# Kernel tuning notes

Measured on AMD Instinct MI355X. Metric: run time of the kernel, lower is better.

Reference implementation:

```python
import jax, jax.numpy as jnp
import numpy as np

B = 65536      # batch
E = 4          # experts per node
F = 32         # per-node input features
H = 256        # hidden width
NODES = 4
D_MID = 128    # intermediate node output dim
D_OUT = 8      # final head dim


def _lin_w(k, fan_in, fan_out):
    b = 1.0 / np.sqrt(fan_in)
    return jax.random.uniform(k, (E, fan_in, fan_out), jnp.float32, -b, b)


def setup_inputs() -> dict:
    key = jax.random.key(0)
    ks = jax.random.split(key, 8)
    feats = jax.random.normal(ks[0], (B, NODES * F), dtype=jnp.float32)
    # routing one-hot blocks embedded in the input vector (as the module expects)
    ohs = [jax.nn.one_hot(jax.random.randint(ks[1 + j], (B,), 0, E), E, dtype=jnp.float32)
           for j in range(NODES)]
    input_val = jnp.concatenate([feats] + ohs, axis=1)  # [B, 144]
    p = {"input_val": input_val}
    kc = iter(jax.random.split(ks[5], 32))
    # node 0: no pre-interface; post: F->H relu, H->D_MID relu
    p["W0_0"] = _lin_w(next(kc), F, H); p["b0_0"] = jnp.full((E, H), 0.1, jnp.float32)
    p["W0_1"] = _lin_w(next(kc), H, D_MID); p["b0_1"] = jnp.full((E, D_MID), 0.1, jnp.float32)
    # nodes 1,2: pre F->H relu; post (D_MID+H)->H relu, H->D_MID relu
    for j in (1, 2):
        p[f"W{j}_pre"] = _lin_w(next(kc), F, H); p[f"b{j}_pre"] = jnp.full((E, H), 0.1, jnp.float32)
        p[f"W{j}_0"] = _lin_w(next(kc), D_MID + H, H); p[f"b{j}_0"] = jnp.full((E, H), 0.1, jnp.float32)
        p[f"W{j}_1"] = _lin_w(next(kc), H, D_MID); p[f"b{j}_1"] = jnp.full((E, D_MID), 0.1, jnp.float32)
    # node 3 (output): pre F->H relu; post (D_MID+H)->H relu, H->D_OUT identity
    p["W3_pre"] = _lin_w(next(kc), F, H); p["b3_pre"] = jnp.full((E, H), 0.1, jnp.float32)
    p["W3_0"] = _lin_w(next(kc), D_MID + H, H); p["b3_0"] = jnp.full((E, H), 0.1, jnp.float32)
    p["W3_1"] = jax.random.uniform(next(kc), (E, H, D_OUT), jnp.float32, -0.003, 0.003)
    p["b3_1"] = jax.random.uniform(next(kc), (E, D_OUT), jnp.float32, -0.003, 0.003)
    return p


def reference(input_val, W0_0, b0_0, W0_1, b0_1,
              W1_pre, b1_pre, W1_0, b1_0, W1_1, b1_1,
              W2_pre, b2_pre, W2_0, b2_0, W2_1, b2_1,
              W3_pre, b3_pre, W3_0, b3_0, W3_1, b3_1):
    relu = jax.nn.relu
    xs = [input_val[:, j * F:(j + 1) * F] for j in range(NODES)]          # per-node features
    ohs = [input_val[:, NODES * F + j * E: NODES * F + (j + 1) * E] for j in range(NODES)]

    def combine(oh, outs):  # oh [B,E] exact one-hot; outs [E,B,D] -> exact per-row expert pick
        return jnp.einsum('be,ebo->bo', oh, outs)

    # node 0 (no previous-level input)
    def n0(W0, b0, W1, b1):
        h = relu(xs[0] @ W0 + b0)
        return relu(h @ W1 + b1)
    x = combine(ohs[0], jax.vmap(n0)(W0_0, b0_0, W0_1, b0_1))  # [B, D_MID]

    def node(xj, xprev, relu_last):
        def f(Wp, bp, W0, b0, W1, b1):
            h = relu(xj @ Wp + bp)                      # pre-interface
            h = jnp.concatenate([xprev, h], axis=-1)    # interface: cat(prev, pre)
            h = relu(h @ W0 + b0)
            o = h @ W1 + b1
            return relu(o) if relu_last else o
        return f

    x = combine(ohs[1], jax.vmap(node(xs[1], x, True))(W1_pre, b1_pre, W1_0, b1_0, W1_1, b1_1))
    x = combine(ohs[2], jax.vmap(node(xs[2], x, True))(W2_pre, b2_pre, W2_0, b2_0, W2_1, b2_1))
    x = combine(ohs[3], jax.vmap(node(xs[3], x, False))(W3_pre, b3_pre, W3_0, b3_0, W3_1, b3_1))
    return x  # [B, D_OUT]
```

## Files before the change

kernel.cpp:

```cpp
#include <hip/hip_runtime.h>
#include <hip/hip_bf16.h>
#include <stdint.h>

typedef unsigned int u32;
typedef unsigned short u16;
typedef unsigned char u8;
typedef __bf16 bf16x8 __attribute__((ext_vector_type(8)));
typedef float f32x4 __attribute__((ext_vector_type(4)));

#define NB 65536
#define NBLK 1280
#define PERM_TOT (NBLK * 64)
#define INVR 0xFFFFFFFFu
#define BLK_DEAD 0xFFFFu

#define O_ROWS 0
#define O_XJ   256
#define O_P    (O_XJ + 4096)
#define O_H    (O_P + 16384)
#define O_RED  O_P
#define SM_BYTES (O_H + 32768)

__device__ __host__ constexpr int TS(int m) {
  constexpr int t[12] = {0, 64, 320, 384, 1152, 1408, 1472, 2240, 2496, 2560, 3328, 3360};
  return t[m];
}

__device__ __forceinline__ u16 f2bf(float f) {
  u32 u = __builtin_bit_cast(u32, f);
  u32 r = (u + 0x7FFFu + ((u >> 16) & 1u)) >> 16;
  return (u16)r;
}
__device__ __forceinline__ float relu_f(float x) { return x > 0.f ? x : 0.f; }
__device__ __forceinline__ f32x4 mfma16(bf16x8 a, bf16x8 b, f32x4 c) {
  return __builtin_amdgcn_mfma_f32_16x16x32_bf16(a, b, c, 0, 0, 0);
}

__device__ __forceinline__ void mkpair(f32x4 acc, float bias, bool dorelu, int l16,
                                       u32& w0, u32& w1) {
  float v0 = acc[0] + bias, v1 = acc[1] + bias, v2 = acc[2] + bias, v3 = acc[3] + bias;
  if (dorelu) { v0 = relu_f(v0); v1 = relu_f(v1); v2 = relu_f(v2); v3 = relu_f(v3); }
  u32 a = (u32)f2bf(v0) | ((u32)f2bf(v1) << 16);
  u32 b = (u32)f2bf(v2) | ((u32)f2bf(v3) << 16);
  u32 ax = (u32)__shfl_xor((int)a, 1);
  u32 bx = (u32)__shfl_xor((int)b, 1);
  if ((l16 & 1) == 0) { w0 = (a & 0xffffu) | (ax << 16); w1 = (a >> 16) | (ax & 0xffff0000u); }
  else                { w0 = (bx & 0xffffu) | (b << 16); w1 = (bx >> 16) | (b & 0xffff0000u); }
}

__device__ __forceinline__ void frag_store_pair(char* base, int KT, int m0, int col,
                                                u32 w0, u32 w1) {
  char* d = base + (((m0 >> 4) * KT + (col >> 5)) << 10) +
            (((m0 & 15) + (((col & 31) >> 3) << 4)) << 4) + (col & 7) * 2;
  *(u32*)d = w0; *(u32*)(d + 16) = w1;
}


__global__ void k_init(u32* cnt) { cnt[threadIdx.x] = 0u; }

__global__ void k_route(const float* __restrict__ inp, u8* __restrict__ bkt,
                        u32* __restrict__ cnt) {
  __shared__ u32 h[256];
  const int tid = threadIdx.x;
  h[tid] = 0u;
  __syncthreads();
  const int r = blockIdx.x * 256 + tid;
  const float4* oh = (const float4*)(inp + (size_t)r * 144 + 128);
  u32 b = 0;
#pragma unroll
  for (int j = 0; j < 4; j++) {
    float4 v = oh[j];
    u32 e = v.y > 0.5f ? 1u : (v.z > 0.5f ? 2u : (v.w > 0.5f ? 3u : 0u));
    b |= e << (2 * j);
  }
  bkt[r] = (u8)b;
  atomicAdd(&h[b], 1u);
  __syncthreads();
  atomicAdd(&cnt[tid], h[tid]);
}

__global__ void k_scan(const u32* __restrict__ cnt, u32* __restrict__ cur,
                       u16* __restrict__ blk2b, u32* __restrict__ perm) {
  __shared__ u32 s[256];
  const int tid = threadIdx.x;
  const u32 c = cnt[tid];
  const u32 pad = (c + 63u) & ~63u;
  s[tid] = pad;
  __syncthreads();
  for (int d = 1; d < 256; d <<= 1) {
    u32 v = (tid >= d) ? s[tid - d] : 0u;
    __syncthreads();
    s[tid] += v;
    __syncthreads();
  }
  const u32 off = s[tid] - pad;
  const u32 total = s[255];
  cur[tid] = off;
  for (u32 i = off + c; i < off + pad; i++) perm[i] = INVR;
  for (u32 blk = off >> 6; blk < (off + pad) >> 6; blk++) blk2b[blk] = (u16)tid;
  for (u32 i = total + tid; i < PERM_TOT; i += 256) perm[i] = INVR;
  for (u32 blk = (total >> 6) + tid; blk < NBLK; blk += 256) blk2b[blk] = BLK_DEAD;
}

__global__ void k_scatter(const u8* __restrict__ bkt, u32* __restrict__ cur,
                          u32* __restrict__ perm) {
  __shared__ u32 h[256], base[256];
  const int tid = threadIdx.x;
  h[tid] = 0u;
  __syncthreads();
  const int r = blockIdx.x * 256 + tid;
  const u32 b = bkt[r];
  const u32 rank = atomicAdd(&h[b], 1u);
  __syncthreads();
  base[tid] = h[tid] ? atomicAdd(&cur[tid], h[tid]) : 0u;
  __syncthreads();
  perm[base[b] + rank] = (u32)r;
}


struct PrepArgs {
  const float* src[11];
  int K[11], Nsrc[11];
  int tileStart[12];
};

__global__ void k_prep(__bf16* __restrict__ pk, PrepArgs pa) {
  const int tid = threadIdx.x;
  const int gt = blockIdx.x * 4 + (tid >> 6);
  const int lane = tid & 63, quad = lane >> 4, l16 = lane & 15;
  int m = 0;
  while (gt >= pa.tileStart[m + 1]) m++;
  const int loc = gt - pa.tileStart[m];
  const int K = pa.K[m], Ns = pa.Nsrc[m];
  const int Np = Ns < 16 ? 16 : Ns;
  const int KT = K >> 5, NT = Np >> 4;
  const int e = loc / (KT * NT), rem = loc % (KT * NT);
  const int nt = rem / KT, kt = rem % KT;
  const int k = kt * 32 + quad * 8, n = nt * 16 + l16;
  u32 hw[4];
  if (n < Ns) {
    const float* s = pa.src[m] + ((size_t)e * K + k) * Ns + n;
    u16 h[8];
#pragma unroll
    for (int j = 0; j < 8; j++) h[j] = f2bf(s[(size_t)j * Ns]);
    hw[0] = (u32)h[0] | ((u32)h[1] << 16);
    hw[1] = (u32)h[2] | ((u32)h[3] << 16);
    hw[2] = (u32)h[4] | ((u32)h[5] << 16);
    hw[3] = (u32)h[6] | ((u32)h[7] << 16);
  } else {
    hw[0] = hw[1] = hw[2] = hw[3] = 0u;
  }
  uint4 w; w.x = hw[0]; w.y = hw[1]; w.z = hw[2]; w.w = hw[3];
  *(uint4*)((char*)pk + (size_t)gt * 1024 + lane * 16) = w;
}


__device__ __forceinline__ void xj_load(const float* inp, u32 myrow, int tid, int node,
                                        float4& v0, float4& v1) {
  v0 = make_float4(0.f, 0.f, 0.f, 0.f); v1 = v0;
  if (myrow != INVR) {
    const int c8 = (tid & 3) << 3;
    const float4* p = (const float4*)(inp + (size_t)myrow * 144 + node * 32 + c8);
    v0 = p[0]; v1 = p[1];
  }
}

__device__ __forceinline__ void xj_store(char* sm, int tid, float4 v0, float4 v1) {
  const int r = tid >> 2;
  uint4 w;
  w.x = (u32)f2bf(v0.x) | ((u32)f2bf(v0.y) << 16);
  w.y = (u32)f2bf(v0.z) | ((u32)f2bf(v0.w) << 16);
  w.z = (u32)f2bf(v1.x) | ((u32)f2bf(v1.y) << 16);
  w.w = (u32)f2bf(v1.z) | ((u32)f2bf(v1.w) << 16);
  *(uint4*)(sm + O_XJ + ((r >> 4) << 10) + ((((tid & 3) << 4) + (r & 15)) << 4)) = w;
}

__device__ __forceinline__ void pre_gemm(char* sm, u32 e, int wave, int lane,
                                         const __bf16* Wp, const float* bp) {
  const int l16 = lane & 15;
  const int wn0 = wave * 64;
  const int rsel = ((lane >> 4) << 2) + ((l16 & 1) ? 2 : 0);
  const int colp = l16 & ~1;
  float bias[4];
#pragma unroll
  for (int nt = 0; nt < 4; nt++) bias[nt] = bp[(size_t)e * 256 + wn0 + nt * 16 + l16];
  f32x4 acc[4][4];
#pragma unroll
  for (int i = 0; i < 4; i++)
#pragma unroll
    for (int j = 0; j < 4; j++) acc[i][j] = (f32x4){0.f, 0.f, 0.f, 0.f};
  bf16x8 a[4], b[4];
#pragma unroll
  for (int nt = 0; nt < 4; nt++)
    b[nt] = *(const bf16x8*)(Wp + (size_t)(e * 16 + (wn0 >> 4) + nt) * 512 + lane * 8);
#pragma unroll
  for (int mt = 0; mt < 4; mt++)
    a[mt] = *(const bf16x8*)(sm + O_XJ + (mt << 10) + lane * 16);
#pragma unroll
  for (int mt = 0; mt < 4; mt++)
#pragma unroll
    for (int nt = 0; nt < 4; nt++) acc[mt][nt] = mfma16(a[mt], b[nt], acc[mt][nt]);
#pragma unroll
  for (int nt = 0; nt < 4; nt++) {
    const int n = wn0 + nt * 16;
#pragma unroll
    for (int mt = 0; mt < 4; mt++) {
      u32 w0, w1;
      mkpair(acc[mt][nt], bias[nt], true, l16, w0, w1);
      frag_store_pair(sm + O_H, 8, mt * 16 + rsel, n + colp, w0, w1);
    }
  }
}

__device__ __forceinline__ void main_gemm(char* sm, u32 e, int wave, int lane,
                                          const __bf16* Wm, const float* bm) {
  const int l16 = lane & 15;
  const int wn0 = wave * 64;
  const int rsel = ((lane >> 4) << 2) + ((l16 & 1) ? 2 : 0);
  const int colp = l16 & ~1;
  float bias[4];
#pragma unroll
  for (int nt = 0; nt < 4; nt++) bias[nt] = bm[(size_t)e * 256 + wn0 + nt * 16 + l16];
  f32x4 acc[4][4];
#pragma unroll
  for (int i = 0; i < 4; i++)
#pragma unroll
    for (int j = 0; j < 4; j++) acc[i][j] = (f32x4){0.f, 0.f, 0.f, 0.f};
  const __bf16* bB = Wm + (size_t)(e * 16 + (wn0 >> 4)) * 12 * 512 + lane * 8;
  bf16x8 bb[2][4];
#pragma unroll
  for (int nt = 0; nt < 4; nt++) {
    bb[0][nt] = *(const bf16x8*)(bB + (size_t)(nt * 12 + 0) * 512);
    bb[1][nt] = *(const bf16x8*)(bB + (size_t)(nt * 12 + 1) * 512);
  }
#pragma unroll
  for (int kt = 0; kt < 12; kt++) {
    bf16x8 a[4];
#pragma unroll
    for (int mt = 0; mt < 4; mt++) {
      a[mt] = (kt < 4)
          ? *(const bf16x8*)(sm + O_P + ((mt * 4 + kt) << 10) + lane * 16)
          : *(const bf16x8*)(sm + O_H + ((mt * 8 + (kt - 4)) << 10) + lane * 16);
    }
#pragma unroll
    for (int mt = 0; mt < 4; mt++)
#pragma unroll
      for (int nt = 0; nt < 4; nt++) acc[mt][nt] = mfma16(a[mt], bb[kt & 1][nt], acc[mt][nt]);
    if (kt < 10) {
#pragma unroll
      for (int nt = 0; nt < 4; nt++)
        bb[kt & 1][nt] = *(const bf16x8*)(bB + (size_t)(nt * 12 + kt + 2) * 512);
    }
  }
  __syncthreads();
#pragma unroll
  for (int nt = 0; nt < 4; nt++) {
    const int n = wn0 + nt * 16;
#pragma unroll
    for (int mt = 0; mt < 4; mt++) {
      u32 w0, w1;
      mkpair(acc[mt][nt], bias[nt], true, l16, w0, w1);
      frag_store_pair(sm + O_H, 8, mt * 16 + rsel, n + colp, w0, w1);
    }
  }
  __syncthreads();
}

__device__ __forceinline__ void out_gemm(char* sm, u32 e, int wave, int lane,
                                         const __bf16* Wo, const float* bo) {
  const int l16 = lane & 15;
  const int on0 = wave * 32;
  const int rsel = ((lane >> 4) << 2) + ((l16 & 1) ? 2 : 0);
  const int colp = l16 & ~1;
  float bias[2];
#pragma unroll
  for (int nt = 0; nt < 2; nt++) bias[nt] = bo[(size_t)e * 128 + on0 + nt * 16 + l16];
  f32x4 acc[4][2];
#pragma unroll
  for (int i = 0; i < 4; i++) { acc[i][0] = (f32x4){0.f,0.f,0.f,0.f}; acc[i][1] = acc[i][0]; }
  const __bf16* bB = Wo + (size_t)(e * 8 + (on0 >> 4)) * 8 * 512 + lane * 8;
  bf16x8 bb[2][2];
#pragma unroll
  for (int nt = 0; nt < 2; nt++) {
    bb[0][nt] = *(const bf16x8*)(bB + (size_t)(nt * 8 + 0) * 512);
    bb[1][nt] = *(const bf16x8*)(bB + (size_t)(nt * 8 + 1) * 512);
  }
#pragma unroll
  for (int kt = 0; kt < 8; kt++) {
    bf16x8 a[4];
#pragma unroll
    for (int mt = 0; mt < 4; mt++)
      a[mt] = *(const bf16x8*)(sm + O_H + ((mt * 8 + kt) << 10) + lane * 16);
#pragma unroll
    for (int mt = 0; mt < 4; mt++)
#pragma unroll
      for (int nt = 0; nt < 2; nt++) acc[mt][nt] = mfma16(a[mt], bb[kt & 1][nt], acc[mt][nt]);
    if (kt < 6) {
#pragma unroll
      for (int nt = 0; nt < 2; nt++)
        bb[kt & 1][nt] = *(const bf16x8*)(bB + (size_t)(nt * 8 + kt + 2) * 512);
    }
  }
#pragma unroll
  for (int nt = 0; nt < 2; nt++) {
    const int n = on0 + nt * 16;
#pragma unroll
    for (int mt = 0; mt < 4; mt++) {
      u32 w0, w1;
      mkpair(acc[mt][nt], bias[nt], true, l16, w0, w1);
      frag_store_pair(sm + O_P, 4, mt * 16 + rsel, n + colp, w0, w1);
    }
  }
}

__global__ __launch_bounds__(256, 3) void fused_k(
    const float* __restrict__ inp, const u32* __restrict__ perm,
    const u16* __restrict__ blk2b, const __bf16* __restrict__ pk,
    const float* __restrict__ b0_0, const float* __restrict__ b0_1,
    const float* __restrict__ b1_p, const float* __restrict__ b1_0,
    const float* __restrict__ b1_1, const float* __restrict__ b2_p,
    const float* __restrict__ b2_0, const float* __restrict__ b2_1,
    const float* __restrict__ b3_p, const float* __restrict__ b3_0,
    const float* __restrict__ b3_1, float* __restrict__ dout) {
  const u32 b = blk2b[blockIdx.x];
  if (b == BLK_DEAD) return;
  __shared__ __align__(16) char sm[SM_BYTES];
  u32* rows = (u32*)sm;
  const int tid = threadIdx.x;
  const int wave = tid >> 6, lane = tid & 63, quad = lane >> 4, l16 = lane & 15;
  if (tid < 64) rows[tid] = perm[blockIdx.x * 64 + tid];
  const u32 e0 = b & 3u, e1 = (b >> 2) & 3u, e2 = (b >> 4) & 3u, e3 = (b >> 6) & 3u;
  __syncthreads();
  const u32 myrow = rows[tid >> 2];

  float4 v0, v1;
  xj_load(inp, myrow, tid, 0, v0, v1);
  xj_store(sm, tid, v0, v1);
  __syncthreads();
  pre_gemm(sm, e0, wave, lane, pk + (size_t)TS(0) * 512, b0_0);
  __syncthreads();
  xj_load(inp, myrow, tid, 1, v0, v1);
  out_gemm(sm, e0, wave, lane, pk + (size_t)TS(1) * 512, b0_1);
  xj_store(sm, tid, v0, v1);
  __syncthreads();
  pre_gemm(sm, e1, wave, lane, pk + (size_t)TS(2) * 512, b1_p);
  __syncthreads();
  main_gemm(sm, e1, wave, lane, pk + (size_t)TS(3) * 512, b1_0);
  xj_load(inp, myrow, tid, 2, v0, v1);
  out_gemm(sm, e1, wave, lane, pk + (size_t)TS(4) * 512, b1_1);
  xj_store(sm, tid, v0, v1);
  __syncthreads();
  pre_gemm(sm, e2, wave, lane, pk + (size_t)TS(5) * 512, b2_p);
  __syncthreads();
  main_gemm(sm, e2, wave, lane, pk + (size_t)TS(6) * 512, b2_0);
  xj_load(inp, myrow, tid, 3, v0, v1);
  out_gemm(sm, e2, wave, lane, pk + (size_t)TS(7) * 512, b2_1);
  xj_store(sm, tid, v0, v1);
  __syncthreads();
  pre_gemm(sm, e3, wave, lane, pk + (size_t)TS(8) * 512, b3_p);
  __syncthreads();
  main_gemm(sm, e3, wave, lane, pk + (size_t)TS(9) * 512, b3_0);

  {
    const __bf16* Wo3 = pk + (size_t)TS(10) * 512;
    f32x4 acc3[4];
#pragma unroll
    for (int i = 0; i < 4; i++) acc3[i] = (f32x4){0.f, 0.f, 0.f, 0.f};
#pragma unroll
    for (int kk = 0; kk < 2; kk++) {
      const int kt = wave * 2 + kk;
      bf16x8 b3 = *(const bf16x8*)(Wo3 + (size_t)(e3 * 8 + kt) * 512 + lane * 8);
      bf16x8 a[4];
#pragma unroll
      for (int mt = 0; mt < 4; mt++)
        a[mt] = *(const bf16x8*)(sm + O_H + ((mt * 8 + kt) << 10) + lane * 16);
#pragma unroll
      for (int mt = 0; mt < 4; mt++) acc3[mt] = mfma16(a[mt], b3, acc3[mt]);
    }
#pragma unroll
    for (int mt = 0; mt < 4; mt++)
#pragma unroll
      for (int r = 0; r < 4; r++)
        *(float*)(sm + O_RED +
                  (((size_t)wave * 64 + mt * 16 + quad * 4 + r) * 16 + l16) * 4) = acc3[mt][r];
    __syncthreads();
    const int m = tid >> 2, c = (tid & 3) * 2;
    float s0 = 0.f, s1 = 0.f;
#pragma unroll
    for (int w = 0; w < 4; w++) {
      s0 += *(float*)(sm + O_RED + (((size_t)w * 64 + m) * 16 + c) * 4);
      s1 += *(float*)(sm + O_RED + (((size_t)w * 64 + m) * 16 + c + 1) * 4);
    }
    if (myrow != INVR) {
      float2 o;
      o.x = s0 + b3_1[(size_t)e3 * 8 + c];
      o.y = s1 + b3_1[(size_t)e3 * 8 + c + 1];
      *(float2*)(dout + (size_t)myrow * 8 + c) = o;
    }
  }
}


extern "C" void kernel_launch(void* const* d_in, const int* in_sizes, int n_in,
                              void* d_out, int out_size, void* d_ws, size_t ws_size,
                              hipStream_t stream) {
  (void)in_sizes; (void)n_in; (void)out_size; (void)ws_size;
  const float* inp = (const float*)d_in[0];
  char* ws = (char*)d_ws;

  const size_t oCNT = 0;
  const size_t oCUR = 1024;
  const size_t oBKT = 2048;
  const size_t oB2B = oBKT + NB;
  const size_t oPERM = (oB2B + NBLK * 2 + 255) & ~(size_t)255;
  const size_t oPK = (oPERM + (size_t)PERM_TOT * 4 + 255) & ~(size_t)255;

  u32* cnt = (u32*)(ws + oCNT);
  u32* cur = (u32*)(ws + oCUR);
  u8* bkt = (u8*)(ws + oBKT);
  u16* blk2b = (u16*)(ws + oB2B);
  u32* perm = (u32*)(ws + oPERM);
  __bf16* pk = (__bf16*)(ws + oPK);

  PrepArgs pa;
  const int widx[11] = {1, 3, 5, 7, 9, 11, 13, 15, 17, 19, 21};
  const int Ks[11] = {32, 256, 32, 384, 256, 32, 384, 256, 32, 384, 256};
  const int Ns[11] = {256, 128, 256, 256, 128, 256, 256, 128, 256, 256, 8};
  for (int m = 0; m < 11; m++) {
    pa.src[m] = (const float*)d_in[widx[m]];
    pa.K[m] = Ks[m]; pa.Nsrc[m] = Ns[m]; pa.tileStart[m] = TS(m);
  }
  pa.tileStart[11] = TS(11);

  hipLaunchKernelGGL(k_init, dim3(1), dim3(256), 0, stream, cnt);
  hipLaunchKernelGGL(k_prep, dim3(TS(11) / 4), dim3(256), 0, stream, pk, pa);
  hipLaunchKernelGGL(k_route, dim3(NB / 256), dim3(256), 0, stream, inp, bkt, cnt);
  hipLaunchKernelGGL(k_scan, dim3(1), dim3(256), 0, stream, cnt, cur, blk2b, perm);
  hipLaunchKernelGGL(k_scatter, dim3(NB / 256), dim3(256), 0, stream, bkt, cur, perm);

  fused_k<<<NBLK, 256, 0, stream>>>(
      inp, perm, blk2b, pk,
      (const float*)d_in[2], (const float*)d_in[4],
      (const float*)d_in[6], (const float*)d_in[8], (const float*)d_in[10],
      (const float*)d_in[12], (const float*)d_in[14], (const float*)d_in[16],
      (const float*)d_in[18], (const float*)d_in[20], (const float*)d_in[22],
      (float*)d_out);
}
```

Measured before the change: 227.2 us.

## Merge routing, weight packing, scan and scatter into two kernels

Replaces the five pre-processing launches (init, prep, route, scan, scatter) with two kernels. k_front computes routing buckets and per-block histograms into a 256x256 count table, and packs the weights into bf16 tiles within the same grid. k_place has every block redo the column-sum and prefix scan over that table, then scatter rows into the permutation using a global atomic counter. The goal is to cut launch and serialization overhead from the single-block scan and init kernels. The cost is redundant reduction work: every block reads the full 256 KB count table. The perm tail beyond the padded total is no longer filled with invalid markers, which relies on dead-block skipping in the fused kernel.

```diff
diff --git a/kernel.cpp b/kernel.cpp
--- a/kernel.cpp
+++ b/kernel.cpp
@@ -56,78 +56,15 @@
 }
 
 
-__global__ void k_init(u32* cnt) { cnt[threadIdx.x] = 0u; }
-
-__global__ void k_route(const float* __restrict__ inp, u8* __restrict__ bkt,
-                        u32* __restrict__ cnt) {
-  __shared__ u32 h[256];
-  const int tid = threadIdx.x;
-  h[tid] = 0u;
-  __syncthreads();
-  const int r = blockIdx.x * 256 + tid;
-  const float4* oh = (const float4*)(inp + (size_t)r * 144 + 128);
-  u32 b = 0;
-#pragma unroll
-  for (int j = 0; j < 4; j++) {
-    float4 v = oh[j];
-    u32 e = v.y > 0.5f ? 1u : (v.z > 0.5f ? 2u : (v.w > 0.5f ? 3u : 0u));
-    b |= e << (2 * j);
-  }
-  bkt[r] = (u8)b;
-  atomicAdd(&h[b], 1u);
-  __syncthreads();
-  atomicAdd(&cnt[tid], h[tid]);
-}
-
-__global__ void k_scan(const u32* __restrict__ cnt, u32* __restrict__ cur,
-                       u16* __restrict__ blk2b, u32* __restrict__ perm) {
-  __shared__ u32 s[256];
-  const int tid = threadIdx.x;
-  const u32 c = cnt[tid];
-  const u32 pad = (c + 63u) & ~63u;
-  s[tid] = pad;
-  __syncthreads();
-  for (int d = 1; d < 256; d <<= 1) {
-    u32 v = (tid >= d) ? s[tid - d] : 0u;
-    __syncthreads();
-    s[tid] += v;
-    __syncthreads();
-  }
-  const u32 off = s[tid] - pad;
-  const u32 total = s[255];
-  cur[tid] = off;
-  for (u32 i = off + c; i < off + pad; i++) perm[i] = INVR;
-  for (u32 blk = off >> 6; blk < (off + pad) >> 6; blk++) blk2b[blk] = (u16)tid;
-  for (u32 i = total + tid; i < PERM_TOT; i += 256) perm[i] = INVR;
-  for (u32 blk = (total >> 6) + tid; blk < NBLK; blk += 256) blk2b[blk] = BLK_DEAD;
-}
-
-__global__ void k_scatter(const u8* __restrict__ bkt, u32* __restrict__ cur,
-                          u32* __restrict__ perm) {
-  __shared__ u32 h[256], base[256];
-  const int tid = threadIdx.x;
-  h[tid] = 0u;
-  __syncthreads();
-  const int r = blockIdx.x * 256 + tid;
-  const u32 b = bkt[r];
-  const u32 rank = atomicAdd(&h[b], 1u);
-  __syncthreads();
-  base[tid] = h[tid] ? atomicAdd(&cur[tid], h[tid]) : 0u;
-  __syncthreads();
-  perm[base[b] + rank] = (u32)r;
-}
-
-
 struct PrepArgs {
   const float* src[11];
   int K[11], Nsrc[11];
   int tileStart[12];
 };
 
-__global__ void k_prep(__bf16* __restrict__ pk, PrepArgs pa) {
-  const int tid = threadIdx.x;
-  const int gt = blockIdx.x * 4 + (tid >> 6);
-  const int lane = tid & 63, quad = lane >> 4, l16 = lane & 15;
+__device__ __forceinline__ void prep_tile_dev(__bf16* __restrict__ pk, const PrepArgs& pa,
+                                              int gt, int lane) {
+  const int quad = lane >> 4, l16 = lane & 15;
   int m = 0;
   while (gt >= pa.tileStart[m + 1]) m++;
   const int loc = gt - pa.tileStart[m];
@@ -152,6 +89,73 @@
   }
   uint4 w; w.x = hw[0]; w.y = hw[1]; w.z = hw[2]; w.w = hw[3];
   *(uint4*)((char*)pk + (size_t)gt * 1024 + lane * 16) = w;
+}
+
+
+__global__ __launch_bounds__(256) void k_front(const float* __restrict__ inp,
+                                               u8* __restrict__ bkt,
+                                               u32* __restrict__ cnt2,
+                                               u32* __restrict__ rank,
+                                               __bf16* __restrict__ pk, PrepArgs pa) {
+  __shared__ u32 h[256];
+  const int tid = threadIdx.x;
+  if (blockIdx.x == 0) rank[tid] = 0u;
+  h[tid] = 0u;
+  __syncthreads();
+  const int r = blockIdx.x * 256 + tid;
+  const float4* oh = (const float4*)(inp + (size_t)r * 144 + 128);
+  u32 b = 0;
+#pragma unroll
+  for (int j = 0; j < 4; j++) {
+    float4 v = oh[j];
+    u32 e = v.y > 0.5f ? 1u : (v.z > 0.5f ? 2u : (v.w > 0.5f ? 3u : 0u));
+    b |= e << (2 * j);
+  }
+  bkt[r] = (u8)b;
+  atomicAdd(&h[b], 1u);
+  __syncthreads();
+  cnt2[blockIdx.x * 256 + tid] = h[tid];
+  for (int g4 = blockIdx.x; g4 < TS(11) / 4; g4 += 256)
+    prep_tile_dev(pk, pa, g4 * 4 + (tid >> 6), tid & 63);
+}
+
+
+__global__ __launch_bounds__(256) void k_place(const u8* __restrict__ bkt,
+                                               const u32* __restrict__ cnt2,
+                                               u32* __restrict__ rank,
+                                               u16* __restrict__ blk2b,
+                                               u32* __restrict__ perm) {
+  __shared__ u32 s[256], base[256];
+  const int tid = threadIdx.x;
+  u32 c = 0;
+#pragma unroll 8
+  for (int j = 0; j < 256; j++) c += cnt2[j * 256 + tid];
+  const u32 pad = (c + 63u) & ~63u;
+  s[tid] = pad;
+  __syncthreads();
+  for (int d = 1; d < 256; d <<= 1) {
+    u32 v = (tid >= d) ? s[tid - d] : 0u;
+    __syncthreads();
+    s[tid] += v;
+    __syncthreads();
+  }
+  const u32 off = s[tid] - pad;
+  const u32 total = s[255];
+  __syncthreads();
+  if (blockIdx.x == 0) {
+    for (u32 i = off + c; i < off + pad; i++) perm[i] = INVR;
+    for (u32 blk = off >> 6; blk < (off + pad) >> 6; blk++) blk2b[blk] = (u16)tid;
+    for (u32 blk = (total >> 6) + tid; blk < NBLK; blk += 256) blk2b[blk] = BLK_DEAD;
+  }
+  s[tid] = 0u;
+  __syncthreads();
+  const int r = blockIdx.x * 256 + tid;
+  const u32 b = bkt[r];
+  const u32 lrk = atomicAdd(&s[b], 1u);
+  __syncthreads();
+  base[tid] = off + (s[tid] ? atomicAdd(&rank[tid], s[tid]) : 0u);
+  __syncthreads();
+  perm[base[b] + lrk] = (u32)r;
 }
 
 
@@ -408,17 +412,17 @@
   const float* inp = (const float*)d_in[0];
   char* ws = (char*)d_ws;
 
-  const size_t oCNT = 0;
-  const size_t oCUR = 1024;
-  const size_t oBKT = 2048;
-  const size_t oB2B = oBKT + NB;
-  const size_t oPERM = (oB2B + NBLK * 2 + 255) & ~(size_t)255;
+  const size_t oBKT = 0;
+  const size_t oRANK = oBKT + NB;
+  const size_t oB2B = oRANK + 1024;
+  const size_t oCNT2 = (oB2B + NBLK * 2 + 255) & ~(size_t)255;
+  const size_t oPERM = oCNT2 + 256 * 256 * 4;
   const size_t oPK = (oPERM + (size_t)PERM_TOT * 4 + 255) & ~(size_t)255;
 
-  u32* cnt = (u32*)(ws + oCNT);
-  u32* cur = (u32*)(ws + oCUR);
   u8* bkt = (u8*)(ws + oBKT);
+  u32* rank = (u32*)(ws + oRANK);
   u16* blk2b = (u16*)(ws + oB2B);
+  u32* cnt2 = (u32*)(ws + oCNT2);
   u32* perm = (u32*)(ws + oPERM);
   __bf16* pk = (__bf16*)(ws + oPK);
 
@@ -432,12 +436,10 @@
   }
   pa.tileStart[11] = TS(11);
 
-  hipLaunchKernelGGL(k_init, dim3(1), dim3(256), 0, stream, cnt);
-  hipLaunchKernelGGL(k_prep, dim3(TS(11) / 4), dim3(256), 0, stream, pk, pa);
-  hipLaunchKernelGGL(k_route, dim3(NB / 256), dim3(256), 0, stream, inp, bkt, cnt);
-  hipLaunchKernelGGL(k_scan, dim3(1), dim3(256), 0, stream, cnt, cur, blk2b, perm);
-  hipLaunchKernelGGL(k_scatter, dim3(NB / 256), dim3(256), 0, stream, bkt, cur, perm);
-
+  hipLaunchKernelGGL(k_front, dim3(NB / 256), dim3(256), 0, stream,
+                     inp, bkt, cnt2, rank, pk, pa);
+  hipLaunchKernelGGL(k_place, dim3(NB / 256), dim3(256), 0, stream,
+                     bkt, cnt2, rank, blk2b, perm);
   fused_k<<<NBLK, 256, 0, stream>>>(
       inp, perm, blk2b, pk,
       (const float*)d_in[2], (const float*)d_in[4],
```

Measured after the change: 224.6 us. About the same (-1.2%).
